# Performance work log

Hardware: AMD Instinct MI355X
Metric: run time of the kernel (lower is better)

## Reference

```python
import jax, jax.numpy as jnp
import numpy as np

EPS = 1e-12  # F.normalize default eps

def _l2norm(a, axis):
    n = jnp.sqrt(jnp.sum(a * a, axis=axis, keepdims=True))
    return a / jnp.maximum(n, EPS)

def setup_inputs() -> dict:
    key = jax.random.key(0)
    kx, kc = jax.random.split(key)
    x = jax.random.normal(kx, (32, 64, 64, 64), dtype=jnp.float32)        # [B,C,H,W]
    codebook = 0.2 * jax.random.normal(kc, (512, 64), dtype=jnp.float32)  # nn.init.normal_(w, 0, 0.2)
    return {"x": x, "codebook": codebook}

def reference(x, codebook):
    # mode == 'angular': normalize codebook rows and x along dim=1 (channels)
    cb = _l2norm(codebook, axis=1)          # [K,C]
    xn = _l2norm(x, axis=1)                 # [B,C,H,W]
    # x.transpose(-1, dim) with dim=1 -> swap axes 1 and 3
    xt = jnp.swapaxes(xn, 1, -1)            # [B,W,H,C]
    B, W, H, C = xt.shape
    flat = xt.reshape(-1, C)                # [N,C]
    d = (jnp.sum(cb * cb, axis=1)[None, :]
         + jnp.sum(flat * flat, axis=1, keepdims=True)
         - 2.0 * flat @ cb.T)               # [N,K]
    idx = jnp.argmin(d, axis=1)             # [N]
    codes = cb[idx].reshape(B, W, H, C)
    indices = idx.reshape(B, W, H)
    codes = jnp.swapaxes(codes, 1, -1)      # back to [B,C,H,W]
    indices = jnp.swapaxes(indices, 1, -1)  # [B,H,W]
    return codes, indices
```

## Files before the change

kernel.cpp:

```cpp
#include <hip/hip_runtime.h>

#define VQ_EPS    1e-12f
#define VQ_WINDOW 0.01f
#define VQ_CAP    12

typedef short bf16x8 __attribute__((ext_vector_type(8)));
typedef float f32x4  __attribute__((ext_vector_type(4)));

static __device__ __forceinline__ unsigned short f2bf(float f) {
    unsigned u = __float_as_uint(f);
    u += 0x7fffu + ((u >> 16) & 1u);
    return (unsigned short)(u >> 16);
}

static __device__ __forceinline__ unsigned f2ord(float f) {
    unsigned b = __float_as_uint(f);
    return (b & 0x80000000u) ? ~b : (b | 0x80000000u);
}

static __device__ __forceinline__ void wave_lds_fence() {
    asm volatile("s_waitcnt lgkmcnt(0)" ::: "memory");
}

__global__ __launch_bounds__(64) void cb_prep_kernel(const float* __restrict__ cb,
                                                     float* __restrict__ cbn,
                                                     unsigned short* __restrict__ cbB,
                                                     float* __restrict__ kn2,
                                                     float* __restrict__ kn2p) {
    const int k = blockIdx.x;
    const int c = threadIdx.x;
    float v = cb[k * 64 + c];
    float s = v * v;
    #pragma unroll
    for (int off = 32; off > 0; off >>= 1) s += __shfl_xor(s, off, 64);
    float n = sqrtf(s);
    float cn = v / fmaxf(n, VQ_EPS);
    cbn[k * 64 + c] = cn;

    const int ntile = k >> 4, col = k & 15;
    const int ks = c >> 5, quad = (c >> 3) & 3, j = c & 7;
    cbB[(((ntile * 2 + ks) * 64) + quad * 16 + col) * 8 + j] = f2bf(cn);

    float s2 = cn * cn;
    #pragma unroll
    for (int off = 32; off > 0; off >>= 1) s2 += __shfl_xor(s2, off, 64);
    if (c == 0) { kn2[k] = s2; kn2p[k] = s2 + 2.0f; }
}

__global__ __launch_bounds__(512, 4) void vq_mfma_kernel(const float* __restrict__ x,
                                                      const float* __restrict__ cbn,
                                                      const unsigned short* __restrict__ cbB,
                                                      const float* __restrict__ kn2,
                                                      const float* __restrict__ kn2p,
                                                      float* __restrict__ codes,
                                                      float* __restrict__ idxout) {
    __shared__ __align__(16) unsigned short lcb[32768];
    __shared__ unsigned long long spack[256];
    __shared__ int slist[256][VQ_CAP];
    __shared__ int scnt[256];

    const int t    = threadIdx.x;
    const int lane = t & 63;
    const int wid  = t >> 6;
    const int col  = lane & 15;
    const int quad = lane >> 4;
    const int wr   = wid & 3;
    const int grp  = wid >> 2;
    const int wpix = wr * 16 + col;

    const int rw0 = grp * 2;
    const int rw1 = rw0 + 1;
    const int pbase0 = rw0 * 64;
    const int pbase1 = rw1 * 64;
    const int pslot0 = pbase0 + wpix;
    const int pslot1 = pbase1 + wpix;

    const int rowid0 = blockIdx.x * 4 + rw0;
    const int rowid1 = rowid0 + 1;
    const int b0r = rowid0 >> 6, h0 = rowid0 & 63;
    const int b1r = rowid1 >> 6, h1 = rowid1 & 63;
    const float* xblk0 = x + ((size_t)b0r << 18) + (h0 << 6);
    const float* xblk1 = x + ((size_t)b1r << 18) + (h1 << 6);

    if (quad == 0) {
        scnt[pslot0] = 0; spack[pslot0] = 0xFFFFFFFFFFFFFFFFull;
        scnt[pslot1] = 0; spack[pslot1] = 0xFFFFFFFFFFFFFFFFull;
    }

    float xv0[16], xv1[16];
    #pragma unroll
    for (int ks = 0; ks < 2; ++ks)
        #pragma unroll
        for (int j = 0; j < 8; ++j)
            xv0[ks * 8 + j] = xblk0[(size_t)(ks * 32 + quad * 8 + j) * 4096 + wpix];
    #pragma unroll
    for (int ks = 0; ks < 2; ++ks)
        #pragma unroll
        for (int j = 0; j < 8; ++j)
            xv1[ks * 8 + j] = xblk1[(size_t)(ks * 32 + quad * 8 + j) * 4096 + wpix];

    {
        const uint4* g4 = (const uint4*)cbB;
        uint4*       l4 = (uint4*)lcb;
        #pragma unroll
        for (int r = 0; r < 8; ++r) l4[r * 512 + t] = g4[r * 512 + t];
    }

    __syncthreads();

    float ssp0 = 0.0f, ssp1 = 0.0f;
    #pragma unroll
    for (int i = 0; i < 16; ++i) ssp0 = fmaf(xv0[i], xv0[i], ssp0);
    #pragma unroll
    for (int i = 0; i < 16; ++i) ssp1 = fmaf(xv1[i], xv1[i], ssp1);
    ssp0 += __shfl_xor(ssp0, 16);
    ssp0 += __shfl_xor(ssp0, 32);
    ssp1 += __shfl_xor(ssp1, 16);
    ssp1 += __shfl_xor(ssp1, 32);
    const float m2a0 = -2.0f * (1.0f / fmaxf(sqrtf(ssp0), VQ_EPS));
    const float m2a1 = -2.0f * (1.0f / fmaxf(sqrtf(ssp1), VQ_EPS));
    float m2r0[4], m2r1[4];
    #pragma unroll
    for (int r = 0; r < 4; ++r) m2r0[r] = __shfl(m2a0, quad * 4 + r);
    #pragma unroll
    for (int r = 0; r < 4; ++r) m2r1[r] = __shfl(m2a1, quad * 4 + r);
    const float m2P0 = __shfl(m2a0, lane >> 2);
    const float m2P1 = __shfl(m2a1, lane >> 2);

    bf16x8 afrag0[2], afrag1[2];
    #pragma unroll
    for (int ks = 0; ks < 2; ++ks)
        #pragma unroll
        for (int j = 0; j < 8; ++j) {
            ((unsigned short*)&afrag0[ks])[j] = f2bf(xv0[ks * 8 + j]);
            ((unsigned short*)&afrag1[ks])[j] = f2bf(xv1[ks * 8 + j]);
        }

    const bf16x8* lBf = (const bf16x8*)lcb;

    unsigned run1_0[4] = {0xFFFFFFFFu, 0xFFFFFFFFu, 0xFFFFFFFFu, 0xFFFFFFFFu};
    unsigned run2_0[4] = {0xFFFFFFFFu, 0xFFFFFFFFu, 0xFFFFFFFFu, 0xFFFFFFFFu};
    unsigned run1_1[4] = {0xFFFFFFFFu, 0xFFFFFFFFu, 0xFFFFFFFFu, 0xFFFFFFFFu};
    unsigned run2_1[4] = {0xFFFFFFFFu, 0xFFFFFFFFu, 0xFFFFFFFFu, 0xFFFFFFFFu};
    #pragma unroll 2
    for (int nt = 0; nt < 32; ++nt) {
        bf16x8 b0 = lBf[(nt * 2 + 0) * 64 + lane];
        bf16x8 b1 = lBf[(nt * 2 + 1) * 64 + lane];
        f32x4 c0 = {0.0f, 0.0f, 0.0f, 0.0f};
        f32x4 c1 = {0.0f, 0.0f, 0.0f, 0.0f};
        c0 = __builtin_amdgcn_mfma_f32_16x16x32_bf16(afrag0[0], b0, c0, 0, 0, 0);
        c1 = __builtin_amdgcn_mfma_f32_16x16x32_bf16(afrag1[0], b0, c1, 0, 0, 0);
        c0 = __builtin_amdgcn_mfma_f32_16x16x32_bf16(afrag0[1], b1, c0, 0, 0, 0);
        c1 = __builtin_amdgcn_mfma_f32_16x16x32_bf16(afrag1[1], b1, c1, 0, 0, 0);
        const float    kn   = kn2p[nt * 16 + col];
        const unsigned kidx = (unsigned)(nt * 16 + col);
        #pragma unroll
        for (int r = 0; r < 4; ++r) {
            float s0 = fmaf(m2r0[r], c0[r], kn);
            unsigned key0 = (__float_as_uint(s0) & 0xFFFFFE00u) | kidx;
            unsigned mx0  = max(run1_0[r], key0);
            run1_0[r] = min(run1_0[r], key0);
            run2_0[r] = min(run2_0[r], mx0);
            float s1 = fmaf(m2r1[r], c1[r], kn);
            unsigned key1 = (__float_as_uint(s1) & 0xFFFFFE00u) | kidx;
            unsigned mx1  = max(run1_1[r], key1);
            run1_1[r] = min(run1_1[r], key1);
            run2_1[r] = min(run2_1[r], mx1);
        }
    }

    float thr0[4], thr1[4];
    #pragma unroll
    for (int r = 0; r < 4; ++r) {
        unsigned v = run1_0[r];
        v = min(v, (unsigned)__shfl_xor((int)v, 1));
        v = min(v, (unsigned)__shfl_xor((int)v, 2));
        v = min(v, (unsigned)__shfl_xor((int)v, 4));
        v = min(v, (unsigned)__shfl_xor((int)v, 8));
        thr0[r] = __uint_as_float(v & 0xFFFFFE00u) + VQ_WINDOW;
        unsigned w = run1_1[r];
        w = min(w, (unsigned)__shfl_xor((int)w, 1));
        w = min(w, (unsigned)__shfl_xor((int)w, 2));
        w = min(w, (unsigned)__shfl_xor((int)w, 4));
        w = min(w, (unsigned)__shfl_xor((int)w, 8));
        thr1[r] = __uint_as_float(w & 0xFFFFFE00u) + VQ_WINDOW;
    }

    bool f = false;
    #pragma unroll
    for (int r = 0; r < 4; ++r) {
        f |= (__uint_as_float(run2_0[r] & 0xFFFFFE00u) <= thr0[r]);
        f |= (__uint_as_float(run2_1[r] & 0xFFFFFE00u) <= thr1[r]);
    }
    const unsigned long long waveflag = __ballot(f);

    if (waveflag != 0ull) {
        #pragma unroll 2
        for (int nt = 0; nt < 32; ++nt) {
            bf16x8 b0 = lBf[(nt * 2 + 0) * 64 + lane];
            bf16x8 b1 = lBf[(nt * 2 + 1) * 64 + lane];
            f32x4 c0 = {0.0f, 0.0f, 0.0f, 0.0f};
            f32x4 c1 = {0.0f, 0.0f, 0.0f, 0.0f};
            c0 = __builtin_amdgcn_mfma_f32_16x16x32_bf16(afrag0[0], b0, c0, 0, 0, 0);
            c1 = __builtin_amdgcn_mfma_f32_16x16x32_bf16(afrag1[0], b0, c1, 0, 0, 0);
            c0 = __builtin_amdgcn_mfma_f32_16x16x32_bf16(afrag0[1], b1, c0, 0, 0, 0);
            c1 = __builtin_amdgcn_mfma_f32_16x16x32_bf16(afrag1[1], b1, c1, 0, 0, 0);
            const float kn   = kn2p[nt * 16 + col];
            const int   kidx = nt * 16 + col;
            #pragma unroll
            for (int r = 0; r < 4; ++r) {
                float s0 = fmaf(m2r0[r], c0[r], kn);
                if (s0 <= thr0[r]) {
                    int pix = pbase0 + wr * 16 + quad * 4 + r;
                    int pos = atomicAdd(&scnt[pix], 1);
                    if (pos < VQ_CAP) slist[pix][pos] = kidx;
                }
                float s1 = fmaf(m2r1[r], c1[r], kn);
                if (s1 <= thr1[r]) {
                    int pix = pbase1 + wr * 16 + quad * 4 + r;
                    int pos = atomicAdd(&scnt[pix], 1);
                    if (pos < VQ_CAP) slist[pix][pos] = kidx;
                }
            }
        }
    } else {
        #pragma unroll
        for (int r = 0; r < 4; ++r) {
            float s0 = __uint_as_float(run1_0[r] & 0xFFFFFE00u);
            if (s0 <= thr0[r]) {
                int pix = pbase0 + wr * 16 + quad * 4 + r;
                int pos = atomicAdd(&scnt[pix], 1);
                if (pos < VQ_CAP) slist[pix][pos] = (int)(run1_0[r] & 0x1FFu);
            }
            float s1 = __uint_as_float(run1_1[r] & 0xFFFFFE00u);
            if (s1 <= thr1[r]) {
                int pix = pbase1 + wr * 16 + quad * 4 + r;
                int pos = atomicAdd(&scnt[pix], 1);
                if (pos < VQ_CAP) slist[pix][pos] = (int)(run1_1[r] & 0x1FFu);
            }
        }
    }
    wave_lds_fence();

    {
        const int pw  = wr * 16 + (lane >> 2);
        const int sub = lane & 3;
        {
            const int P   = pbase0 + pw;
            const int cnt = scnt[P];
            if (cnt > 1) {
                const float* xp = xblk0 + pw;
                if (cnt <= VQ_CAP) {
                    for (int i = sub; i < cnt; i += 4) {
                        const int k = slist[P][i];
                        const float* cr = cbn + (size_t)k * 64;
                        float dot = 0.0f;
                        #pragma unroll 8
                        for (int c = 0; c < 64; ++c)
                            dot = fmaf(xp[(size_t)c * 4096], cr[c], dot);
                        float s = fmaf(m2P0, dot, kn2[k]);
                        unsigned long long key =
                            ((unsigned long long)f2ord(s) << 32) | (unsigned)k;
                        atomicMin(&spack[P], key);
                    }
                } else {
                    for (int k = sub; k < 512; k += 4) {
                        const float* cr = cbn + (size_t)k * 64;
                        float dot = 0.0f;
                        #pragma unroll 8
                        for (int c = 0; c < 64; ++c)
                            dot = fmaf(xp[(size_t)c * 4096], cr[c], dot);
                        float s = fmaf(m2P0, dot, kn2[k]);
                        unsigned long long key =
                            ((unsigned long long)f2ord(s) << 32) | (unsigned)k;
                        atomicMin(&spack[P], key);
                    }
                }
            }
        }
        {
            const int P   = pbase1 + pw;
            const int cnt = scnt[P];
            if (cnt > 1) {
                const float* xp = xblk1 + pw;
                if (cnt <= VQ_CAP) {
                    for (int i = sub; i < cnt; i += 4) {
                        const int k = slist[P][i];
                        const float* cr = cbn + (size_t)k * 64;
                        float dot = 0.0f;
                        #pragma unroll 8
                        for (int c = 0; c < 64; ++c)
                            dot = fmaf(xp[(size_t)c * 4096], cr[c], dot);
                        float s = fmaf(m2P1, dot, kn2[k]);
                        unsigned long long key =
                            ((unsigned long long)f2ord(s) << 32) | (unsigned)k;
                        atomicMin(&spack[P], key);
                    }
                } else {
                    for (int k = sub; k < 512; k += 4) {
                        const float* cr = cbn + (size_t)k * 64;
                        float dot = 0.0f;
                        #pragma unroll 8
                        for (int c = 0; c < 64; ++c)
                            dot = fmaf(xp[(size_t)c * 4096], cr[c], dot);
                        float s = fmaf(m2P1, dot, kn2[k]);
                        unsigned long long key =
                            ((unsigned long long)f2ord(s) << 32) | (unsigned)k;
                        atomicMin(&spack[P], key);
                    }
                }
            }
        }
    }
    wave_lds_fence();

    {
        const int cntw = scnt[pslot0];
        const int bk = (cntw == 1) ? slist[pslot0][0]
                                   : (int)(spack[pslot0] & 0xFFFFFFFFull);
        if (quad == 0) idxout[rowid0 * 64 + wpix] = (float)bk;
        const float4* crow = (const float4*)(cbn + (size_t)bk * 64) + quad * 4;
        float* cp = codes + ((size_t)b0r << 18) + (h0 << 6) + wpix;
        #pragma unroll
        for (int q = 0; q < 4; ++q) {
            float4 v = crow[q];
            const int c0 = quad * 16 + q * 4;
            cp[(size_t)(c0 + 0) * 4096] = v.x;
            cp[(size_t)(c0 + 1) * 4096] = v.y;
            cp[(size_t)(c0 + 2) * 4096] = v.z;
            cp[(size_t)(c0 + 3) * 4096] = v.w;
        }
    }
    {
        const int cntw = scnt[pslot1];
        const int bk = (cntw == 1) ? slist[pslot1][0]
                                   : (int)(spack[pslot1] & 0xFFFFFFFFull);
        if (quad == 0) idxout[rowid1 * 64 + wpix] = (float)bk;
        const float4* crow = (const float4*)(cbn + (size_t)bk * 64) + quad * 4;
        float* cp = codes + ((size_t)b1r << 18) + (h1 << 6) + wpix;
        #pragma unroll
        for (int q = 0; q < 4; ++q) {
            float4 v = crow[q];
            const int c0 = quad * 16 + q * 4;
            cp[(size_t)(c0 + 0) * 4096] = v.x;
            cp[(size_t)(c0 + 1) * 4096] = v.y;
            cp[(size_t)(c0 + 2) * 4096] = v.z;
            cp[(size_t)(c0 + 3) * 4096] = v.w;
        }
    }
}

extern "C" void kernel_launch(void* const* d_in, const int* in_sizes, int n_in,
                              void* d_out, int out_size, void* d_ws, size_t ws_size,
                              hipStream_t stream) {
    const float* x  = (const float*)d_in[0];
    const float* cb = (const float*)d_in[1];

    float*          cbn  = (float*)d_ws;
    unsigned short* cbB  = (unsigned short*)(cbn + 512 * 64);
    float*          kn2  = (float*)(cbB + 32768);
    float*          kn2p = kn2 + 512;

    float* codes  = (float*)d_out;
    float* idxout = codes + (size_t)32 * 64 * 64 * 64;

    cb_prep_kernel<<<512, 64, 0, stream>>>(cb, cbn, cbB, kn2, kn2p);
    vq_mfma_kernel<<<512, 512, 0, stream>>>(x, cbn, cbB, kn2, kn2p, codes, idxout);
}
```

Measured before the change: 122.8 us.

## Use 1024-thread blocks, stagger codebook tile order, split rescan per row

Each block now has 1024 threads and covers 8 image rows, so the 64KB bf16 codebook copy into LDS is amortized over twice as many pixels. The per-pixel candidate lists become unsigned short with a smaller cap to fit the extra slots in LDS. Each wave starts its codebook walk at a different tile offset to spread LDS bank accesses. The second MFMA pass that collects near-tie candidates is now decided separately for each of a wave's two rows, so a row with no near-ties skips its recompute. Risks are lower occupancy with 1024-thread blocks and only 256 blocks in the grid, and more overflow into the slow path with the smaller cap.

```diff
diff --git a/kernel.cpp b/kernel.cpp
--- a/kernel.cpp
+++ b/kernel.cpp
@@ -2,7 +2,7 @@
 
 #define VQ_EPS    1e-12f
 #define VQ_WINDOW 0.01f
-#define VQ_CAP    12
+#define VQ_CAP    10
 
 typedef short bf16x8 __attribute__((ext_vector_type(8)));
 typedef float f32x4  __attribute__((ext_vector_type(4)));
@@ -47,7 +47,7 @@
     if (c == 0) { kn2[k] = s2; kn2p[k] = s2 + 2.0f; }
 }
 
-__global__ __launch_bounds__(512, 4) void vq_mfma_kernel(const float* __restrict__ x,
+__global__ __launch_bounds__(1024, 8) void vq_mfma_kernel(const float* __restrict__ x,
                                                       const float* __restrict__ cbn,
                                                       const unsigned short* __restrict__ cbB,
                                                       const float* __restrict__ kn2,
@@ -55,9 +55,9 @@
                                                       float* __restrict__ codes,
                                                       float* __restrict__ idxout) {
     __shared__ __align__(16) unsigned short lcb[32768];
-    __shared__ unsigned long long spack[256];
-    __shared__ int slist[256][VQ_CAP];
-    __shared__ int scnt[256];
+    __shared__ unsigned long long spack[512];
+    __shared__ unsigned short slist[512][VQ_CAP];
+    __shared__ int scnt[512];
 
     const int t    = threadIdx.x;
     const int lane = t & 63;
@@ -69,13 +69,12 @@
     const int wpix = wr * 16 + col;
 
     const int rw0 = grp * 2;
-    const int rw1 = rw0 + 1;
     const int pbase0 = rw0 * 64;
-    const int pbase1 = rw1 * 64;
+    const int pbase1 = pbase0 + 64;
     const int pslot0 = pbase0 + wpix;
     const int pslot1 = pbase1 + wpix;
 
-    const int rowid0 = blockIdx.x * 4 + rw0;
+    const int rowid0 = blockIdx.x * 8 + rw0;
     const int rowid1 = rowid0 + 1;
     const int b0r = rowid0 >> 6, h0 = rowid0 & 63;
     const int b1r = rowid1 >> 6, h1 = rowid1 & 63;
@@ -103,7 +102,7 @@
         const uint4* g4 = (const uint4*)cbB;
         uint4*       l4 = (uint4*)lcb;
         #pragma unroll
-        for (int r = 0; r < 8; ++r) l4[r * 512 + t] = g4[r * 512 + t];
+        for (int r = 0; r < 4; ++r) l4[r * 1024 + t] = g4[r * 1024 + t];
     }
 
     __syncthreads();
@@ -137,6 +136,7 @@
         }
 
     const bf16x8* lBf = (const bf16x8*)lcb;
+    const int ntoff = wr * 8;
 
     unsigned run1_0[4] = {0xFFFFFFFFu, 0xFFFFFFFFu, 0xFFFFFFFFu, 0xFFFFFFFFu};
     unsigned run2_0[4] = {0xFFFFFFFFu, 0xFFFFFFFFu, 0xFFFFFFFFu, 0xFFFFFFFFu};
@@ -144,16 +144,17 @@
     unsigned run2_1[4] = {0xFFFFFFFFu, 0xFFFFFFFFu, 0xFFFFFFFFu, 0xFFFFFFFFu};
     #pragma unroll 2
     for (int nt = 0; nt < 32; ++nt) {
-        bf16x8 b0 = lBf[(nt * 2 + 0) * 64 + lane];
-        bf16x8 b1 = lBf[(nt * 2 + 1) * 64 + lane];
+        const int ntr = (nt + ntoff) & 31;
+        bf16x8 b0 = lBf[(ntr * 2 + 0) * 64 + lane];
+        bf16x8 b1 = lBf[(ntr * 2 + 1) * 64 + lane];
         f32x4 c0 = {0.0f, 0.0f, 0.0f, 0.0f};
         f32x4 c1 = {0.0f, 0.0f, 0.0f, 0.0f};
         c0 = __builtin_amdgcn_mfma_f32_16x16x32_bf16(afrag0[0], b0, c0, 0, 0, 0);
         c1 = __builtin_amdgcn_mfma_f32_16x16x32_bf16(afrag1[0], b0, c1, 0, 0, 0);
         c0 = __builtin_amdgcn_mfma_f32_16x16x32_bf16(afrag0[1], b1, c0, 0, 0, 0);
         c1 = __builtin_amdgcn_mfma_f32_16x16x32_bf16(afrag1[1], b1, c1, 0, 0, 0);
-        const float    kn   = kn2p[nt * 16 + col];
-        const unsigned kidx = (unsigned)(nt * 16 + col);
+        const float    kn   = kn2p[ntr * 16 + col];
+        const unsigned kidx = (unsigned)(ntr * 16 + col);
         #pragma unroll
         for (int r = 0; r < 4; ++r) {
             float s0 = fmaf(m2r0[r], c0[r], kn);
@@ -186,57 +187,72 @@
         thr1[r] = __uint_as_float(w & 0xFFFFFE00u) + VQ_WINDOW;
     }
 
-    bool f = false;
+    bool f0 = false, f1 = false;
     #pragma unroll
     for (int r = 0; r < 4; ++r) {
-        f |= (__uint_as_float(run2_0[r] & 0xFFFFFE00u) <= thr0[r]);
-        f |= (__uint_as_float(run2_1[r] & 0xFFFFFE00u) <= thr1[r]);
-    }
-    const unsigned long long waveflag = __ballot(f);
-
-    if (waveflag != 0ull) {
+        f0 |= (__uint_as_float(run2_0[r] & 0xFFFFFE00u) <= thr0[r]);
+        f1 |= (__uint_as_float(run2_1[r] & 0xFFFFFE00u) <= thr1[r]);
+    }
+    const bool f0w = (__ballot(f0) != 0ull);
+    const bool f1w = (__ballot(f1) != 0ull);
+
+    if (f0w || f1w) {
         #pragma unroll 2
         for (int nt = 0; nt < 32; ++nt) {
-            bf16x8 b0 = lBf[(nt * 2 + 0) * 64 + lane];
-            bf16x8 b1 = lBf[(nt * 2 + 1) * 64 + lane];
-            f32x4 c0 = {0.0f, 0.0f, 0.0f, 0.0f};
-            f32x4 c1 = {0.0f, 0.0f, 0.0f, 0.0f};
-            c0 = __builtin_amdgcn_mfma_f32_16x16x32_bf16(afrag0[0], b0, c0, 0, 0, 0);
-            c1 = __builtin_amdgcn_mfma_f32_16x16x32_bf16(afrag1[0], b0, c1, 0, 0, 0);
-            c0 = __builtin_amdgcn_mfma_f32_16x16x32_bf16(afrag0[1], b1, c0, 0, 0, 0);
-            c1 = __builtin_amdgcn_mfma_f32_16x16x32_bf16(afrag1[1], b1, c1, 0, 0, 0);
-            const float kn   = kn2p[nt * 16 + col];
-            const int   kidx = nt * 16 + col;
-            #pragma unroll
-            for (int r = 0; r < 4; ++r) {
-                float s0 = fmaf(m2r0[r], c0[r], kn);
-                if (s0 <= thr0[r]) {
-                    int pix = pbase0 + wr * 16 + quad * 4 + r;
-                    int pos = atomicAdd(&scnt[pix], 1);
-                    if (pos < VQ_CAP) slist[pix][pos] = kidx;
+            const int ntr = (nt + ntoff) & 31;
+            bf16x8 b0 = lBf[(ntr * 2 + 0) * 64 + lane];
+            bf16x8 b1 = lBf[(ntr * 2 + 1) * 64 + lane];
+            const float kn   = kn2p[ntr * 16 + col];
+            const int   kidx = ntr * 16 + col;
+            if (f0w) {
+                f32x4 c0 = {0.0f, 0.0f, 0.0f, 0.0f};
+                c0 = __builtin_amdgcn_mfma_f32_16x16x32_bf16(afrag0[0], b0, c0, 0, 0, 0);
+                c0 = __builtin_amdgcn_mfma_f32_16x16x32_bf16(afrag0[1], b1, c0, 0, 0, 0);
+                #pragma unroll
+                for (int r = 0; r < 4; ++r) {
+                    float s0 = fmaf(m2r0[r], c0[r], kn);
+                    if (s0 <= thr0[r]) {
+                        int pix = pbase0 + wr * 16 + quad * 4 + r;
+                        int pos = atomicAdd(&scnt[pix], 1);
+                        if (pos < VQ_CAP) slist[pix][pos] = (unsigned short)kidx;
+                    }
                 }
-                float s1 = fmaf(m2r1[r], c1[r], kn);
-                if (s1 <= thr1[r]) {
-                    int pix = pbase1 + wr * 16 + quad * 4 + r;
-                    int pos = atomicAdd(&scnt[pix], 1);
-                    if (pos < VQ_CAP) slist[pix][pos] = kidx;
+            }
+            if (f1w) {
+                f32x4 c1 = {0.0f, 0.0f, 0.0f, 0.0f};
+                c1 = __builtin_amdgcn_mfma_f32_16x16x32_bf16(afrag1[0], b0, c1, 0, 0, 0);
+                c1 = __builtin_amdgcn_mfma_f32_16x16x32_bf16(afrag1[1], b1, c1, 0, 0, 0);
+                #pragma unroll
+                for (int r = 0; r < 4; ++r) {
+                    float s1 = fmaf(m2r1[r], c1[r], kn);
+                    if (s1 <= thr1[r]) {
+                        int pix = pbase1 + wr * 16 + quad * 4 + r;
+                        int pos = atomicAdd(&scnt[pix], 1);
+                        if (pos < VQ_CAP) slist[pix][pos] = (unsigned short)kidx;
+                    }
                 }
             }
         }
-    } else {
+    }
+    if (!f0w) {
         #pragma unroll
         for (int r = 0; r < 4; ++r) {
             float s0 = __uint_as_float(run1_0[r] & 0xFFFFFE00u);
             if (s0 <= thr0[r]) {
                 int pix = pbase0 + wr * 16 + quad * 4 + r;
                 int pos = atomicAdd(&scnt[pix], 1);
-                if (pos < VQ_CAP) slist[pix][pos] = (int)(run1_0[r] & 0x1FFu);
-            }
+                if (pos < VQ_CAP) slist[pix][pos] = (unsigned short)(run1_0[r] & 0x1FFu);
+            }
+        }
+    }
+    if (!f1w) {
+        #pragma unroll
+        for (int r = 0; r < 4; ++r) {
             float s1 = __uint_as_float(run1_1[r] & 0xFFFFFE00u);
             if (s1 <= thr1[r]) {
                 int pix = pbase1 + wr * 16 + quad * 4 + r;
                 int pos = atomicAdd(&scnt[pix], 1);
-                if (pos < VQ_CAP) slist[pix][pos] = (int)(run1_1[r] & 0x1FFu);
+                if (pos < VQ_CAP) slist[pix][pos] = (unsigned short)(run1_1[r] & 0x1FFu);
             }
         }
     }
@@ -316,7 +332,7 @@
 
     {
         const int cntw = scnt[pslot0];
-        const int bk = (cntw == 1) ? slist[pslot0][0]
+        const int bk = (cntw == 1) ? (int)slist[pslot0][0]
                                    : (int)(spack[pslot0] & 0xFFFFFFFFull);
         if (quad == 0) idxout[rowid0 * 64 + wpix] = (float)bk;
         const float4* crow = (const float4*)(cbn + (size_t)bk * 64) + quad * 4;
@@ -333,7 +349,7 @@
     }
     {
         const int cntw = scnt[pslot1];
-        const int bk = (cntw == 1) ? slist[pslot1][0]
+        const int bk = (cntw == 1) ? (int)slist[pslot1][0]
                                    : (int)(spack[pslot1] & 0xFFFFFFFFull);
         if (quad == 0) idxout[rowid1 * 64 + wpix] = (float)bk;
         const float4* crow = (const float4*)(cbn + (size_t)bk * 64) + quad * 4;
@@ -365,5 +381,5 @@
     float* idxout = codes + (size_t)32 * 64 * 64 * 64;
 
     cb_prep_kernel<<<512, 64, 0, stream>>>(cb, cbn, cbB, kn2, kn2p);
-    vq_mfma_kernel<<<512, 512, 0, stream>>>(x, cbn, cbB, kn2, kn2p, codes, idxout);
-}
+    vq_mfma_kernel<<<256, 1024, 0, stream>>>(x, cbn, cbB, kn2, kn2p, codes, idxout);
+}
```

Result: slower. 176.8 us (+44.0%).
